# Optimization experiments

Hardware: AMD Instinct MI355X
Metric: run time of the kernel (lower is better)

## Reference

```python
import jax, jax.numpy as jnp
import numpy as np

N_LOC, C, A, H, X, STEPS = 500000, 128, 24, 256, 128, 4


def setup_inputs() -> dict:
    key = jax.random.key(0)
    ks = jax.random.split(key, 12)
    def rn(i, shape, scale=0.05):
        return jax.random.normal(ks[i], shape, dtype=jnp.float32) * scale
    return {
        "x": jax.random.normal(ks[0], (1, X), dtype=jnp.float32),
        "h0": jnp.zeros((1, H), jnp.float32),
        "memory_contents": rn(1, (N_LOC, C), 0.01),
        "memory_addresses": rn(2, (N_LOC, A), 0.1),
        "W_query": rn(3, (H, A + C)),
        "b_query": jnp.zeros((A + C,), jnp.float32),
        "u_sharpen": rn(4, (H,)),
        "b_sharpen": jnp.zeros((1,), jnp.float32),
        "W_erase": rn(5, (H, C)),
        "b_erase": jnp.zeros((C,), jnp.float32),
        "W_cand_h": rn(6, (H, C)),
        "W_cand_x": rn(7, (X, C)),
        "b_cand": jnp.zeros((C,), jnp.float32),
        "W_ih": rn(8, (X + C, 3 * H)),
        "W_hh": rn(9, (H, 3 * H)),
        "b_ih": jnp.zeros((3 * H,), jnp.float32),
        "b_hh": jnp.zeros((3 * H,), jnp.float32),
        "num_addressing_steps": STEPS,
    }


def _gru_cell(inp, h, W_ih, W_hh, b_ih, b_hh):
    # torch.nn.GRUCell semantics
    gi = inp @ W_ih + b_ih  # (1, 3H)
    gh = h @ W_hh + b_hh    # (1, 3H)
    i_r, i_z, i_n = jnp.split(gi, 3, axis=-1)
    h_r, h_z, h_n = jnp.split(gh, 3, axis=-1)
    r = jax.nn.sigmoid(i_r + h_r)
    z = jax.nn.sigmoid(i_z + h_z)
    n = jnp.tanh(i_n + r * h_n)
    return (1.0 - z) * n + z * h


def reference(x, h0, memory_contents, memory_addresses, W_query, b_query,
              u_sharpen, b_sharpen, W_erase, b_erase, W_cand_h, W_cand_x,
              b_cand, W_ih, W_hh, b_ih, b_hh, num_addressing_steps):
    h = h0                      # (1, H)
    mem = memory_contents       # (N, C)
    for _ in range(num_addressing_steps):
        # --- content-based addressing over full memory [addresses || contents] ---
        q = h @ W_query + b_query                              # (1, A+C)
        beta = jax.nn.softplus(h @ u_sharpen + b_sharpen) + 1.0  # (1,)
        sim = memory_addresses @ q[0, :A] + mem @ q[0, A:]     # (N,)
        w = jax.nn.softmax(beta[0] * sim)                      # (N,)
        # --- read ---
        content = (w @ mem)[None, :]                           # (1, C)
        # --- controller step ---
        h = _gru_cell(jnp.concatenate([x, content], axis=1), h, W_ih, W_hh, b_ih, b_hh)
        # --- write: erase + candidate ---
        erase = jax.nn.sigmoid(h @ W_erase + b_erase)          # (1, C)
        cand = jax.nn.relu(h @ W_cand_h + x @ W_cand_x + b_cand)  # (1, C)
        mem = mem * (1.0 - w[:, None] * erase) + w[:, None] * cand
    return h
```

## Files before the change

### kernel.cpp

```cpp
#include <hip/hip_runtime.h>
#include <hip/hip_bf16.h>

#define N_LOC 500000
#define C 128
#define A 24
#define AC 152
#define H 256
#define X 128
#define G3 768
#define GRID_BIG 1024

__device__ __forceinline__ float sigmoidf_(float x) { return 1.0f / (1.0f + __expf(-x)); }

template <int NPREV, bool WRITE_E>
__global__ __launch_bounds__(256) void big_pass(
    const float* __restrict__ mem0, const float* __restrict__ addr,
    const float* __restrict__ qacc,
    const float* __restrict__ ehist,
    const float* __restrict__ chist,
    const float* __restrict__ ssum4,
    const float* __restrict__ earr,
    float* __restrict__ enew,
    float* __restrict__ part)
{
    const int lane = threadIdx.x & 31;
    const int rg   = threadIdx.x >> 5;

    const float4 qc = *(const float4*)(qacc + A + 4 * lane);
    float4 qa = make_float4(0.f, 0.f, 0.f, 0.f);
    if (lane < 6) qa = *(const float4*)(qacc + 4 * lane);
    float beta;
    { float t = qacc[AC]; beta = (t > 20.f ? t : log1pf(__expf(t))) + 1.0f; }

    constexpr int NP = (NPREV > 0) ? NPREV : 1;
    float4 er[NP], cd[NP];
    float inv_s[NP];
#pragma unroll
    for (int s = 0; s < NPREV; ++s) {
        float4 et = *(const float4*)(ehist + (s + 1) * C + 4 * lane);
        er[s].x = sigmoidf_(et.x); er[s].y = sigmoidf_(et.y);
        er[s].z = sigmoidf_(et.z); er[s].w = sigmoidf_(et.w);
        float4 ct = *(const float4*)(chist + (s + 1) * C + 4 * lane);
        cd[s].x = fmaxf(ct.x, 0.f); cd[s].y = fmaxf(ct.y, 0.f);
        cd[s].z = fmaxf(ct.z, 0.f); cd[s].w = fmaxf(ct.w, 0.f);
        inv_s[s] = 1.0f / ssum4[s + 1];
    }

    float4 acc = make_float4(0.f, 0.f, 0.f, 0.f);
    float sumloc = 0.f;
    const int stride = gridDim.x * 8;

    for (int i = blockIdx.x * 8 + rg; i < N_LOC; i += stride) {
        float w_s[NP];
#pragma unroll
        for (int s = 0; s < NPREV; ++s)
            w_s[s] = earr[s * N_LOC + i] * inv_s[s];

        float4 m = *(const float4*)(mem0 + (size_t)i * C + 4 * lane);
#pragma unroll
        for (int s = 0; s < NPREV; ++s) {
            float w = w_s[s];
            m.x = m.x * (1.f - w * er[s].x) + w * cd[s].x;
            m.y = m.y * (1.f - w * er[s].y) + w * cd[s].y;
            m.z = m.z * (1.f - w * er[s].z) + w * cd[s].z;
            m.w = m.w * (1.f - w * er[s].w) + w * cd[s].w;
        }

        float s = m.x * qc.x + m.y * qc.y + m.z * qc.z + m.w * qc.w;
        if (lane < 6) {
            float4 a4 = *(const float4*)(addr + (size_t)i * A + 4 * lane);
            s += a4.x * qa.x + a4.y * qa.y + a4.z * qa.z + a4.w * qa.w;
        }
        s += __shfl_xor(s, 1);
        s += __shfl_xor(s, 2);
        s += __shfl_xor(s, 4);
        s += __shfl_xor(s, 8);
        s += __shfl_xor(s, 16);
        float ev = __expf(beta * s);
        if (WRITE_E && lane == 0) enew[i] = ev;
        if (lane == 0) sumloc += ev;
        acc.x += ev * m.x; acc.y += ev * m.y;
        acc.z += ev * m.z; acc.w += ev * m.w;
    }

    __shared__ float sc[8][C];
    __shared__ float ssum[256];
    *(float4*)(&sc[rg][4 * lane]) = acc;
    ssum[threadIdx.x] = sumloc;
    __syncthreads();
    if (threadIdx.x < C) {
        float v = 0.f;
#pragma unroll
        for (int g = 0; g < 8; ++g) v += sc[g][threadIdx.x];
        part[blockIdx.x * 132 + threadIdx.x] = v;
    }
    for (int off = 128; off > 0; off >>= 1) {
        if (threadIdx.x < off) ssum[threadIdx.x] += ssum[threadIdx.x + off];
        __syncthreads();
    }
    if (threadIdx.x == 0) part[blockIdx.x * 132 + C] = ssum[0];
}

__global__ __launch_bounds__(256) void reduce_part(
    const float* __restrict__ part, float* __restrict__ craw,
    float* __restrict__ ssum4, int step)
{
    const int j = blockIdx.x;
    float v = 0.f;
    for (int b = threadIdx.x; b < GRID_BIG; b += 256)
        v += part[b * 132 + j];
    __shared__ float sh[256];
    sh[threadIdx.x] = v;
    __syncthreads();
    for (int off = 128; off > 0; off >>= 1) {
        if (threadIdx.x < off) sh[threadIdx.x] += sh[threadIdx.x + off];
        __syncthreads();
    }
    if (threadIdx.x == 0) {
        craw[j] = sh[0];
        if (j == C) ssum4[step] = sh[0];
    }
}

__global__ __launch_bounds__(256) void prex(
    const float* __restrict__ x, const float* __restrict__ W_ih,
    const float* __restrict__ b_ih, const float* __restrict__ W_cx,
    float* __restrict__ gix, float* __restrict__ candx)
{
    const int tid = threadIdx.x;
    float a0 = 0.f, a1 = 0.f, a2 = 0.f, ac = 0.f;
    const int k0 = blockIdx.x * 8;
    for (int k = k0; k < k0 + 8; ++k) {
        float xk = x[k];
        const float* row = W_ih + (size_t)k * G3;
        a0 += xk * row[tid];
        a1 += xk * row[256 + tid];
        a2 += xk * row[512 + tid];
        if (tid < C) ac += xk * W_cx[k * C + tid];
    }
    const bool b0 = (blockIdx.x == 0);
    atomicAdd(gix + tid,        a0 + (b0 ? b_ih[tid] : 0.f));
    atomicAdd(gix + 256 + tid,  a1 + (b0 ? b_ih[256 + tid] : 0.f));
    atomicAdd(gix + 512 + tid,  a2 + (b0 ? b_ih[512 + tid] : 0.f));
    if (tid < C) atomicAdd(candx + tid, ac);
}

__global__ __launch_bounds__(256) void post(
    const float* __restrict__ h,
    const float* __restrict__ W_er, const float* __restrict__ b_er,
    const float* __restrict__ W_ch, const float* __restrict__ b_cd,
    const float* __restrict__ W_q,  const float* __restrict__ b_q,
    const float* __restrict__ u_sh, const float* __restrict__ b_sh,
    const float* __restrict__ candx,
    float* __restrict__ eslot, float* __restrict__ cslot,
    float* __restrict__ qacc)
{
    const int tid = threadIdx.x;
    float ae = 0.f, ac = 0.f, aq = 0.f, ab = 0.f;
    const int k0 = blockIdx.x * 16;
    for (int k = k0; k < k0 + 16; ++k) {
        float hk = h[k];
        if (tid < C)  { ae += hk * W_er[k * C + tid]; ac += hk * W_ch[k * C + tid]; }
        if (tid < AC)   aq += hk * W_q[k * AC + tid];
        if (tid == 255) ab += hk * u_sh[k];
    }
    const bool b0 = (blockIdx.x == 0);
    if (tid < C) {
        atomicAdd(eslot + tid, ae + (b0 ? b_er[tid] : 0.f));
        atomicAdd(cslot + tid, ac + (b0 ? (candx[tid] + b_cd[tid]) : 0.f));
    }
    if (tid < AC)   atomicAdd(qacc + tid, aq + (b0 ? b_q[tid] : 0.f));
    if (tid == 255) atomicAdd(qacc + AC, ab + (b0 ? b_sh[0] : 0.f));
}

__global__ __launch_bounds__(256) void gates(
    const float* __restrict__ craw, const float* __restrict__ hprev,
    const float* __restrict__ W_ih, const float* __restrict__ W_hh,
    const float* __restrict__ b_hh, const float* __restrict__ gix,
    float* __restrict__ gacc)
{
    const int tid = threadIdx.x;
    const float inv = 1.0f / craw[C];
    float gi0 = 0.f, gi1 = 0.f, gi2 = 0.f, gh0 = 0.f, gh1 = 0.f, gh2 = 0.f;
    const int kc0 = blockIdx.x * 8;
    for (int k = kc0; k < kc0 + 8; ++k) {
        float ck = craw[k] * inv;
        const float* row = W_ih + (size_t)(X + k) * G3;
        gi0 += ck * row[tid]; gi1 += ck * row[256 + tid]; gi2 += ck * row[512 + tid];
    }
    const int kh0 = blockIdx.x * 16;
    for (int k = kh0; k < kh0 + 16; ++k) {
        float hk = hprev[k];
        const float* row = W_hh + (size_t)k * G3;
        gh0 += hk * row[tid]; gh1 += hk * row[256 + tid]; gh2 += hk * row[512 + tid];
    }
    const bool b0 = (blockIdx.x == 0);
    atomicAdd(gacc + tid,              gi0 + (b0 ? gix[tid] : 0.f));
    atomicAdd(gacc + 256 + tid,        gi1 + (b0 ? gix[256 + tid] : 0.f));
    atomicAdd(gacc + 512 + tid,        gi2 + (b0 ? gix[512 + tid] : 0.f));
    atomicAdd(gacc + G3 + tid,         gh0 + (b0 ? b_hh[tid] : 0.f));
    atomicAdd(gacc + G3 + 256 + tid,   gh1 + (b0 ? b_hh[256 + tid] : 0.f));
    atomicAdd(gacc + G3 + 512 + tid,   gh2 + (b0 ? b_hh[512 + tid] : 0.f));
}

__global__ __launch_bounds__(256) void fin(
    float* gacc, const float* __restrict__ hprev,
    float* __restrict__ hout, float* __restrict__ qacc)
{
    const int j = threadIdx.x;
    float ir = gacc[j], iz = gacc[256 + j], in_ = gacc[512 + j];
    float hr = gacc[G3 + j], hz = gacc[G3 + 256 + j], hn = gacc[G3 + 512 + j];
    float r = sigmoidf_(ir + hr);
    float z = sigmoidf_(iz + hz);
    float n = tanhf(in_ + r * hn);
    float hp = hprev[j];
    hout[j] = (1.f - z) * n + z * hp;
    gacc[j] = 0.f; gacc[256 + j] = 0.f; gacc[512 + j] = 0.f;
    gacc[G3 + j] = 0.f; gacc[G3 + 256 + j] = 0.f; gacc[G3 + 512 + j] = 0.f;
    if (j < 160) qacc[j] = 0.f;
}

extern "C" void kernel_launch(void* const* d_in, const int* in_sizes, int n_in,
                              void* d_out, int out_size, void* d_ws, size_t ws_size,
                              hipStream_t stream) {
    (void)in_sizes; (void)n_in; (void)out_size; (void)ws_size;
    const float* x    = (const float*)d_in[0];
    const float* h0   = (const float*)d_in[1];
    const float* mem0 = (const float*)d_in[2];
    const float* addr = (const float*)d_in[3];
    const float* W_q  = (const float*)d_in[4];
    const float* b_q  = (const float*)d_in[5];
    const float* u_sh = (const float*)d_in[6];
    const float* b_sh = (const float*)d_in[7];
    const float* W_er = (const float*)d_in[8];
    const float* b_er = (const float*)d_in[9];
    const float* W_ch = (const float*)d_in[10];
    const float* W_cx = (const float*)d_in[11];
    const float* b_cd = (const float*)d_in[12];
    const float* W_ih = (const float*)d_in[13];
    const float* W_hh = (const float*)d_in[14];
    const float* b_ih = (const float*)d_in[15];
    const float* b_hh = (const float*)d_in[16];
    float* hout = (float*)d_out;

    float* e     = (float*)d_ws;
    float* part  = e + 3 * N_LOC;
    float* S     = part + GRID_BIG * 132;
    float* craw  = S;
    float* gacc  = S + 144;
    float* qacc  = S + 1680;
    float* ehist = S + 1840;
    float* chist = S + 2352;
    float* gix   = S + 2864;
    float* candx = S + 3632;
    float* ssum4 = S + 3760;

    hipMemsetAsync(S, 0, 3768 * sizeof(float), stream);
    prex<<<16, 256, 0, stream>>>(x, W_ih, b_ih, W_cx, gix, candx);
    post<<<16, 256, 0, stream>>>(h0, W_er, b_er, W_ch, b_cd, W_q, b_q, u_sh, b_sh,
                                 candx, ehist, chist, qacc);
    big_pass<0, true><<<GRID_BIG, 256, 0, stream>>>(mem0, addr, qacc, ehist, chist,
                                                    ssum4, e, e, part);
    reduce_part<<<129, 256, 0, stream>>>(part, craw, ssum4, 1);

    gates<<<16, 256, 0, stream>>>(craw, h0, W_ih, W_hh, b_hh, gix, gacc);
    fin<<<1, 256, 0, stream>>>(gacc, h0, hout, qacc);
    post<<<16, 256, 0, stream>>>(hout, W_er, b_er, W_ch, b_cd, W_q, b_q, u_sh, b_sh,
                                 candx, ehist + C, chist + C, qacc);
    big_pass<1, true><<<GRID_BIG, 256, 0, stream>>>(mem0, addr, qacc, ehist, chist,
                                                    ssum4, e, e + N_LOC, part);
    reduce_part<<<129, 256, 0, stream>>>(part, craw, ssum4, 2);

    gates<<<16, 256, 0, stream>>>(craw, hout, W_ih, W_hh, b_hh, gix, gacc);
    fin<<<1, 256, 0, stream>>>(gacc, hout, hout, qacc);
    post<<<16, 256, 0, stream>>>(hout, W_er, b_er, W_ch, b_cd, W_q, b_q, u_sh, b_sh,
                                 candx, ehist + 2 * C, chist + 2 * C, qacc);
    big_pass<2, true><<<GRID_BIG, 256, 0, stream>>>(mem0, addr, qacc, ehist, chist,
                                                    ssum4, e, e + 2 * N_LOC, part);
    reduce_part<<<129, 256, 0, stream>>>(part, craw, ssum4, 3);

    gates<<<16, 256, 0, stream>>>(craw, hout, W_ih, W_hh, b_hh, gix, gacc);
    fin<<<1, 256, 0, stream>>>(gacc, hout, hout, qacc);
    post<<<16, 256, 0, stream>>>(hout, W_er, b_er, W_ch, b_cd, W_q, b_q, u_sh, b_sh,
                                 candx, ehist + 3 * C, chist + 3 * C, qacc);
    big_pass<3, false><<<GRID_BIG, 256, 0, stream>>>(mem0, addr, qacc, ehist, chist,
                                                     ssum4, e, e, part);
    reduce_part<<<129, 256, 0, stream>>>(part, craw, ssum4, 4);

    gates<<<16, 256, 0, stream>>>(craw, hout, W_ih, W_hh, b_hh, gix, gacc);
    fin<<<1, 256, 0, stream>>>(gacc, hout, hout, qacc);
}
```

Measured before the change: 825.9 us.

## Cache memory as bf16 on first pass and fuse gates with GRU finish

The first big pass converts the fp32 memory contents and addresses to bf16 copies in workspace, and the later passes stream those half-size copies. This cuts HBM read traffic across steps at the cost of extra writes in pass 0 and lower precision in the similarity and read. The gates and fin kernels are merged: partials go to per-block slots and a last-block counter finishes the GRU, dropping a launch and the atomics.

```diff
diff --git a/kernel.cpp b/kernel.cpp
--- a/kernel.cpp
+++ b/kernel.cpp
@@ -10,11 +10,23 @@
 #define G3 768
 #define GRID_BIG 1024
 
+typedef unsigned short ushort_t;
+
 __device__ __forceinline__ float sigmoidf_(float x) { return 1.0f / (1.0f + __expf(-x)); }
 
-template <int NPREV, bool WRITE_E>
+__device__ __forceinline__ ushort_t f2bf(float f) {
+    unsigned u = __float_as_uint(f);
+    u += 0x7FFFu + ((u >> 16) & 1u);
+    return (ushort_t)(u >> 16);
+}
+__device__ __forceinline__ float bf2f(ushort_t s) {
+    return __uint_as_float(((unsigned)s) << 16);
+}
+
+template <int NPREV, bool WRITE_E, bool CONVERT>
 __global__ __launch_bounds__(256) void big_pass(
     const float* __restrict__ mem0, const float* __restrict__ addr,
+    ushort_t* __restrict__ membf, ushort_t* __restrict__ addrbf,
     const float* __restrict__ qacc,
     const float* __restrict__ ehist,
     const float* __restrict__ chist,
@@ -51,15 +63,30 @@
     const int stride = gridDim.x * 8;
 
     for (int i = blockIdx.x * 8 + rg; i < N_LOC; i += stride) {
-        float w_s[NP];
-#pragma unroll
-        for (int s = 0; s < NPREV; ++s)
-            w_s[s] = earr[s * N_LOC + i] * inv_s[s];
-
-        float4 m = *(const float4*)(mem0 + (size_t)i * C + 4 * lane);
+        float4 m, a4 = make_float4(0.f, 0.f, 0.f, 0.f);
+        if (CONVERT) {
+            m = *(const float4*)(mem0 + (size_t)i * C + 4 * lane);
+            ushort4 mu; mu.x = f2bf(m.x); mu.y = f2bf(m.y);
+            mu.z = f2bf(m.z); mu.w = f2bf(m.w);
+            *(ushort4*)(membf + (size_t)i * C + 4 * lane) = mu;
+            if (lane < 6) {
+                a4 = *(const float4*)(addr + (size_t)i * A + 4 * lane);
+                ushort4 au; au.x = f2bf(a4.x); au.y = f2bf(a4.y);
+                au.z = f2bf(a4.z); au.w = f2bf(a4.w);
+                *(ushort4*)(addrbf + (size_t)i * A + 4 * lane) = au;
+            }
+        } else {
+            ushort4 mu = *(const ushort4*)(membf + (size_t)i * C + 4 * lane);
+            m = make_float4(bf2f(mu.x), bf2f(mu.y), bf2f(mu.z), bf2f(mu.w));
+            if (lane < 6) {
+                ushort4 au = *(const ushort4*)(addrbf + (size_t)i * A + 4 * lane);
+                a4 = make_float4(bf2f(au.x), bf2f(au.y), bf2f(au.z), bf2f(au.w));
+            }
+        }
+
 #pragma unroll
         for (int s = 0; s < NPREV; ++s) {
-            float w = w_s[s];
+            float w = earr[s * N_LOC + i] * inv_s[s];
             m.x = m.x * (1.f - w * er[s].x) + w * cd[s].x;
             m.y = m.y * (1.f - w * er[s].y) + w * cd[s].y;
             m.z = m.z * (1.f - w * er[s].z) + w * cd[s].z;
@@ -67,10 +94,7 @@
         }
 
         float s = m.x * qc.x + m.y * qc.y + m.z * qc.z + m.w * qc.w;
-        if (lane < 6) {
-            float4 a4 = *(const float4*)(addr + (size_t)i * A + 4 * lane);
-            s += a4.x * qa.x + a4.y * qa.y + a4.z * qa.z + a4.w * qa.w;
-        }
+        s += a4.x * qa.x + a4.y * qa.y + a4.z * qa.z + a4.w * qa.w;
         s += __shfl_xor(s, 1);
         s += __shfl_xor(s, 2);
         s += __shfl_xor(s, 4);
@@ -173,11 +197,12 @@
     if (tid == 255) atomicAdd(qacc + AC, ab + (b0 ? b_sh[0] : 0.f));
 }
 
-__global__ __launch_bounds__(256) void gates(
+__global__ __launch_bounds__(256) void gatesfin(
     const float* __restrict__ craw, const float* __restrict__ hprev,
     const float* __restrict__ W_ih, const float* __restrict__ W_hh,
     const float* __restrict__ b_hh, const float* __restrict__ gix,
-    float* __restrict__ gacc)
+    float* __restrict__ p2, float* __restrict__ hout,
+    float* __restrict__ qacc, unsigned* __restrict__ counter)
 {
     const int tid = threadIdx.x;
     const float inv = 1.0f / craw[C];
@@ -195,29 +220,32 @@
         gh0 += hk * row[tid]; gh1 += hk * row[256 + tid]; gh2 += hk * row[512 + tid];
     }
     const bool b0 = (blockIdx.x == 0);
-    atomicAdd(gacc + tid,              gi0 + (b0 ? gix[tid] : 0.f));
-    atomicAdd(gacc + 256 + tid,        gi1 + (b0 ? gix[256 + tid] : 0.f));
-    atomicAdd(gacc + 512 + tid,        gi2 + (b0 ? gix[512 + tid] : 0.f));
-    atomicAdd(gacc + G3 + tid,         gh0 + (b0 ? b_hh[tid] : 0.f));
-    atomicAdd(gacc + G3 + 256 + tid,   gh1 + (b0 ? b_hh[256 + tid] : 0.f));
-    atomicAdd(gacc + G3 + 512 + tid,   gh2 + (b0 ? b_hh[512 + tid] : 0.f));
-}
-
-__global__ __launch_bounds__(256) void fin(
-    float* gacc, const float* __restrict__ hprev,
-    float* __restrict__ hout, float* __restrict__ qacc)
-{
-    const int j = threadIdx.x;
-    float ir = gacc[j], iz = gacc[256 + j], in_ = gacc[512 + j];
-    float hr = gacc[G3 + j], hz = gacc[G3 + 256 + j], hn = gacc[G3 + 512 + j];
+    float* pb = p2 + blockIdx.x * 1536;
+    pb[tid]        = gi0 + (b0 ? gix[tid] : 0.f);
+    pb[256 + tid]  = gi1 + (b0 ? gix[256 + tid] : 0.f);
+    pb[512 + tid]  = gi2 + (b0 ? gix[512 + tid] : 0.f);
+    pb[768 + tid]  = gh0 + (b0 ? b_hh[tid] : 0.f);
+    pb[1024 + tid] = gh1 + (b0 ? b_hh[256 + tid] : 0.f);
+    pb[1280 + tid] = gh2 + (b0 ? b_hh[512 + tid] : 0.f);
+    __threadfence();
+    __syncthreads();
+    __shared__ int lastBlk;
+    if (tid == 0) lastBlk = (atomicAdd(counter, 1u) == 15u) ? 1 : 0;
+    __syncthreads();
+    if (!lastBlk) return;
+    __threadfence();
+    float ir = 0.f, iz = 0.f, in_ = 0.f, hr = 0.f, hz = 0.f, hn = 0.f;
+    for (int b = 0; b < 16; ++b) {
+        const float* q = p2 + b * 1536;
+        ir += q[tid]; iz += q[256 + tid]; in_ += q[512 + tid];
+        hr += q[768 + tid]; hz += q[1024 + tid]; hn += q[1280 + tid];
+    }
     float r = sigmoidf_(ir + hr);
     float z = sigmoidf_(iz + hz);
     float n = tanhf(in_ + r * hn);
-    float hp = hprev[j];
-    hout[j] = (1.f - z) * n + z * hp;
-    gacc[j] = 0.f; gacc[256 + j] = 0.f; gacc[512 + j] = 0.f;
-    gacc[G3 + j] = 0.f; gacc[G3 + 256 + j] = 0.f; gacc[G3 + 512 + j] = 0.f;
-    if (j < 160) qacc[j] = 0.f;
+    hout[tid] = (1.f - z) * n + z * hprev[tid];
+    if (tid < 160) qacc[tid] = 0.f;
+    if (tid == 0) *counter = 0u;
 }
 
 extern "C" void kernel_launch(void* const* d_in, const int* in_sizes, int n_in,
@@ -243,50 +271,49 @@
     const float* b_hh = (const float*)d_in[16];
     float* hout = (float*)d_out;
 
-    float* e     = (float*)d_ws;
-    float* part  = e + 3 * N_LOC;
-    float* S     = part + GRID_BIG * 132;
-    float* craw  = S;
-    float* gacc  = S + 144;
-    float* qacc  = S + 1680;
-    float* ehist = S + 1840;
-    float* chist = S + 2352;
-    float* gix   = S + 2864;
-    float* candx = S + 3632;
-    float* ssum4 = S + 3760;
-
-    hipMemsetAsync(S, 0, 3768 * sizeof(float), stream);
+    float*    e      = (float*)d_ws;
+    ushort_t* membf  = (ushort_t*)(e + 3 * N_LOC);
+    ushort_t* addrbf = membf + (size_t)N_LOC * C;
+    float*    part   = (float*)(addrbf + (size_t)N_LOC * A);
+    float*    S      = part + GRID_BIG * 132;
+    float*    craw   = S;
+    float*    qacc   = S + 144;
+    float*    ehist  = S + 304;
+    float*    chist  = S + 816;
+    float*    gix    = S + 1328;
+    float*    candx  = S + 2096;
+    float*    ssum4  = S + 2224;
+    unsigned* counter= (unsigned*)(S + 2232);
+    float*    p2     = S + 2240;
+
+    hipMemsetAsync(S, 0, 2240 * sizeof(float), stream);
     prex<<<16, 256, 0, stream>>>(x, W_ih, b_ih, W_cx, gix, candx);
     post<<<16, 256, 0, stream>>>(h0, W_er, b_er, W_ch, b_cd, W_q, b_q, u_sh, b_sh,
                                  candx, ehist, chist, qacc);
-    big_pass<0, true><<<GRID_BIG, 256, 0, stream>>>(mem0, addr, qacc, ehist, chist,
-                                                    ssum4, e, e, part);
+    big_pass<0, true, true><<<GRID_BIG, 256, 0, stream>>>(
+        mem0, addr, membf, addrbf, qacc, ehist, chist, ssum4, e, e, part);
     reduce_part<<<129, 256, 0, stream>>>(part, craw, ssum4, 1);
-
-    gates<<<16, 256, 0, stream>>>(craw, h0, W_ih, W_hh, b_hh, gix, gacc);
-    fin<<<1, 256, 0, stream>>>(gacc, h0, hout, qacc);
+    gatesfin<<<16, 256, 0, stream>>>(craw, h0, W_ih, W_hh, b_hh, gix, p2, hout,
+                                     qacc, counter);
     post<<<16, 256, 0, stream>>>(hout, W_er, b_er, W_ch, b_cd, W_q, b_q, u_sh, b_sh,
                                  candx, ehist + C, chist + C, qacc);
-    big_pass<1, true><<<GRID_BIG, 256, 0, stream>>>(mem0, addr, qacc, ehist, chist,
-                                                    ssum4, e, e + N_LOC, part);
+    big_pass<1, true, false><<<GRID_BIG, 256, 0, stream>>>(
+        mem0, addr, membf, addrbf, qacc, ehist, chist, ssum4, e, e + N_LOC, part);
     reduce_part<<<129, 256, 0, stream>>>(part, craw, ssum4, 2);
-
-    gates<<<16, 256, 0, stream>>>(craw, hout, W_ih, W_hh, b_hh, gix, gacc);
-    fin<<<1, 256, 0, stream>>>(gacc, hout, hout, qacc);
+    gatesfin<<<16, 256, 0, stream>>>(craw, hout, W_ih, W_hh, b_hh, gix, p2, hout,
+                                     qacc, counter);
     post<<<16, 256, 0, stream>>>(hout, W_er, b_er, W_ch, b_cd, W_q, b_q, u_sh, b_sh,
                                  candx, ehist + 2 * C, chist + 2 * C, qacc);
-    big_pass<2, true><<<GRID_BIG, 256, 0, stream>>>(mem0, addr, qacc, ehist, chist,
-                                                    ssum4, e, e + 2 * N_LOC, part);
+    big_pass<2, true, false><<<GRID_BIG, 256, 0, stream>>>(
+        mem0, addr, membf, addrbf, qacc, ehist, chist, ssum4, e, e + 2 * N_LOC, part);
     reduce_part<<<129, 256, 0, stream>>>(part, craw, ssum4, 3);
-
-    gates<<<16, 256, 0, stream>>>(craw, hout, W_ih, W_hh, b_hh, gix, gacc);
-    fin<<<1, 256, 0, stream>>>(gacc, hout, hout, qacc);
+    gatesfin<<<16, 256, 0, stream>>>(craw, hout, W_ih, W_hh, b_hh, gix, p2, hout,
+                                     qacc, counter);
     post<<<16, 256, 0, stream>>>(hout, W_er, b_er, W_ch, b_cd, W_q, b_q, u_sh, b_sh,
                                  candx, ehist + 3 * C, chist + 3 * C, qacc);
-    big_pass<3, false><<<GRID_BIG, 256, 0, stream>>>(mem0, addr, qacc, ehist, chist,
-                                                     ssum4, e, e, part);
+    big_pass<3, false, false><<<GRID_BIG, 256, 0, stream>>>(
+        mem0, addr, membf, addrbf, qacc, ehist, chist, ssum4, e, e, part);
     reduce_part<<<129, 256, 0, stream>>>(part, craw, ssum4, 4);
-
-    gates<<<16, 256, 0, stream>>>(craw, hout, W_ih, W_hh, b_hh, gix, gacc);
-    fin<<<1, 256, 0, stream>>>(gacc, hout, hout, qacc);
-}
+    gatesfin<<<16, 256, 0, stream>>>(craw, hout, W_ih, W_hh, b_hh, gix, p2, hout,
+                                     qacc, counter);
+}
```

New measurement: 753.7 us. 8.7% less time.
